# Kernel tuning notes

Measured on AMD Instinct MI355X. Metric: run time of the kernel, lower is better.

Reference implementation:

```python
import jax, jax.numpy as jnp
import numpy as np

N_NODES = 100000
N_EDGES = 1600000
D = 128

def setup_inputs() -> dict:
    key = jax.random.key(0)
    ks = jax.random.split(key, 6)
    x = jax.random.normal(ks[0], (N_NODES, D), dtype=jnp.float32)
    edge_src = jax.random.randint(ks[1], (N_EDGES,), 0, N_NODES, dtype=jnp.int32)
    edge_dst = jax.random.randint(ks[2], (N_EDGES,), 0, N_NODES, dtype=jnp.int32)
    # Glorot-ish scaling for 128x128 linears
    scale = 1.0 / np.sqrt(D)
    W1 = jax.random.normal(ks[3], (D, D), dtype=jnp.float32) * scale
    b1 = jnp.zeros((D,), dtype=jnp.float32)
    W2 = jax.random.normal(ks[4], (D, D), dtype=jnp.float32) * scale
    b2 = jnp.zeros((D,), dtype=jnp.float32)
    return {"x": x, "edge_src": edge_src, "edge_dst": edge_dst,
            "W1": W1, "b1": b1, "W2": W2, "b2": b2}

def reference(x, edge_src, edge_dst, W1, b1, W2, b2):
    # g.set_data('.hidden', data); g.apply(pre_mod): Linear + ReLU per node
    h = jax.nn.relu(x @ W1 + b1)                      # [N, D]
    # g.push(func=sum): each node's hidden becomes the sum of its
    # in-neighbors' hidden features (gather by src, scatter-add by dst).
    msgs = h[edge_src]                                # [E, D] irregular gather
    agg = jax.ops.segment_sum(msgs, edge_dst, num_segments=N_NODES)  # [N, D]
    # g.apply(post_mod): Linear per node; g.pop_data returns result
    out = agg @ W2 + b2                               # [N, D]
    return out
```

## Files before the change

### kernel.cpp

```cpp
#include <hip/hip_runtime.h>

#define D 128
#define NPB 256
#define NBMAX 512
#define BKCAP 8192
#define CHUNK 8192
#define OVF_CAP 8192

typedef __attribute__((ext_vector_type(8))) short short8x;
typedef __attribute__((ext_vector_type(4))) float f32x4;

__device__ inline unsigned int f2bf(float f) {
    unsigned int u = __builtin_bit_cast(unsigned int, f);
    return (u + 0x7fffu + ((u >> 16) & 1u)) >> 16;
}
__device__ inline float bflo(unsigned int v) {
    return __builtin_bit_cast(float, v << 16);
}
__device__ inline float bfhi(unsigned int v) {
    return __builtin_bit_cast(float, v & 0xffff0000u);
}
__device__ inline unsigned int pack2(float lo, float hi) {
    return f2bf(lo) | (f2bf(hi) << 16);
}

__global__ __launch_bounds__(256) void pack_w(
    const float* __restrict__ W1, const float* __restrict__ W2,
    uint4* __restrict__ pack, int* __restrict__ zero_area, int nz)
{
    if (blockIdx.x == 16) {
        for (int i = threadIdx.x; i < nz; i += 256) zero_area[i] = 0;
        return;
    }
    int e = blockIdx.x * 256 + threadIdx.x;
    const float* W = (e & 2048) ? W2 : W1;
    int f = (e >> 6) & 31, l = e & 63;
    int kt = f >> 3, nt = f & 7;
    int k0 = kt * 32 + (l >> 4) * 8;
    int col = nt * 16 + (l & 15);
    unsigned int v[8];
#pragma unroll
    for (int j = 0; j < 8; ++j) v[j] = f2bf(W[(size_t)(k0 + j) * D + col]);
    uint4 o;
    o.x = v[0] | (v[1] << 16);
    o.y = v[2] | (v[3] << 16);
    o.z = v[4] | (v[5] << 16);
    o.w = v[6] | (v[7] << 16);
    pack[e] = o;
}

__global__ __launch_bounds__(256) void build_gemm(
    const int* __restrict__ esrc, const int* __restrict__ edst,
    int* __restrict__ gfill, unsigned* __restrict__ pairs,
    int* __restrict__ ovf_cnt, int2* __restrict__ ovf_list, int E, int NB,
    int nscatter,
    const float* __restrict__ xin, const uint4* __restrict__ wpack,
    const float* __restrict__ b1, uint4* __restrict__ zout4, int n_rows)
{
    __shared__ __align__(16) char smem[65536];
    const int t = threadIdx.x;

    if (blockIdx.x < nscatter) {
        int* lcnt  = (int*)smem;
        int* lbase = lcnt + NBMAX;
        for (int b = t; b < NB; b += 256) lcnt[b] = 0;
        __syncthreads();
        int cb = blockIdx.x * CHUNK;
        int ce = min(E, cb + CHUNK);
        for (int i = cb + t; i < ce; i += 256)
            atomicAdd(&lcnt[edst[i] >> 8], 1);
        __syncthreads();
        for (int b = t; b < NB; b += 256) {
            int c = lcnt[b];
            lbase[b] = c ? atomicAdd(&gfill[b], c) : 0;
            lcnt[b] = 0;
        }
        __syncthreads();
        for (int i = cb + t; i < ce; i += 256) {
            int d = edst[i];
            int s = esrc[i];
            int b = d >> 8;
            int pos = lbase[b] + atomicAdd(&lcnt[b], 1);
            if (pos < BKCAP) {
                pairs[(size_t)b * BKCAP + pos] = ((unsigned)s << 8) | (unsigned)(d & 255);
            } else {
                int o = atomicAdd(ovf_cnt, 1);
                if (o < OVF_CAP) ovf_list[o] = make_int2(s, d);
            }
        }
        return;
    }

    uint4* ws  = (uint4*)smem;
    uint4* xs4 = ws + 2048;
    const int row0 = (blockIdx.x - nscatter) * 128;

#pragma unroll
    for (int i = 0; i < 8; ++i) ws[t + 256 * i] = wpack[t + 256 * i];

    const float4* g = (const float4*)xin;
#pragma unroll
    for (int i = 0; i < 8; ++i) {
        int c = t + 256 * i;
        int row = c >> 4, kc = c & 15;
        int grow = row0 + row;
        if (grow < n_rows) {
            float4 f0 = g[(size_t)grow * 32 + kc * 2];
            float4 f1 = g[(size_t)grow * 32 + kc * 2 + 1];
            uint4 v;
            v.x = pack2(f0.x, f0.y);
            v.y = pack2(f0.z, f0.w);
            v.z = pack2(f1.x, f1.y);
            v.w = pack2(f1.z, f1.w);
            xs4[row * 16 + (kc ^ (row & 7))] = v;
        }
    }
    __syncthreads();

    const int l = t & 63;
    const int w = t >> 6;
    const int l15 = l & 15;
    const int lk = l >> 4;
    const int arow0 = w * 32 + l15;
    const int arow1 = arow0 + 16;

    float bias1[8];
#pragma unroll
    for (int nt = 0; nt < 8; ++nt) bias1[nt] = b1[nt * 16 + l15];

    f32x4 acc1[2][8];
#pragma unroll
    for (int rt = 0; rt < 2; ++rt)
#pragma unroll
        for (int nt = 0; nt < 8; ++nt) acc1[rt][nt] = (f32x4){0.f, 0.f, 0.f, 0.f};

#pragma unroll
    for (int kt = 0; kt < 4; ++kt) {
        int kc0 = kt * 4 + lk;
        short8x a0 = *(const short8x*)&xs4[arow0 * 16 + (kc0 ^ (arow0 & 7))];
        short8x a1 = *(const short8x*)&xs4[arow1 * 16 + (kc0 ^ (arow1 & 7))];
#pragma unroll
        for (int nt = 0; nt < 8; ++nt) {
            short8x bf = *(const short8x*)&ws[(kt * 8 + nt) * 64 + l];
            acc1[0][nt] = __builtin_amdgcn_mfma_f32_16x16x32_bf16(a0, bf, acc1[0][nt], 0, 0, 0);
            acc1[1][nt] = __builtin_amdgcn_mfma_f32_16x16x32_bf16(a1, bf, acc1[1][nt], 0, 0, 0);
        }
    }

    unsigned short* hsu = (unsigned short*)xs4;
#pragma unroll
    for (int rt = 0; rt < 2; ++rt) {
#pragma unroll
        for (int nt = 0; nt < 8; ++nt) {
            int col = nt * 16 + l15;
            int ci = (col >> 3), ce2 = (col & 7);
#pragma unroll
            for (int r = 0; r < 4; ++r) {
                int rowl = w * 32 + rt * 16 + lk * 4 + r;
                float v = fmaxf(acc1[rt][nt][r] + bias1[nt], 0.f);
                hsu[(rowl * 16 + (ci ^ (rowl & 7))) * 8 + ce2] = (unsigned short)f2bf(v);
            }
        }
    }
    __syncthreads();

#pragma unroll
    for (int i = 0; i < 8; ++i) ws[t + 256 * i] = wpack[2048 + t + 256 * i];
    __syncthreads();

    f32x4 acc2[2][8];
#pragma unroll
    for (int rt = 0; rt < 2; ++rt)
#pragma unroll
        for (int nt = 0; nt < 8; ++nt) acc2[rt][nt] = (f32x4){0.f, 0.f, 0.f, 0.f};

#pragma unroll
    for (int kt = 0; kt < 4; ++kt) {
        int kc0 = kt * 4 + lk;
        short8x a0 = *(const short8x*)&xs4[arow0 * 16 + (kc0 ^ (arow0 & 7))];
        short8x a1 = *(const short8x*)&xs4[arow1 * 16 + (kc0 ^ (arow1 & 7))];
#pragma unroll
        for (int nt = 0; nt < 8; ++nt) {
            short8x bf = *(const short8x*)&ws[(kt * 8 + nt) * 64 + l];
            acc2[0][nt] = __builtin_amdgcn_mfma_f32_16x16x32_bf16(a0, bf, acc2[0][nt], 0, 0, 0);
            acc2[1][nt] = __builtin_amdgcn_mfma_f32_16x16x32_bf16(a1, bf, acc2[1][nt], 0, 0, 0);
        }
    }
    __syncthreads();

    unsigned short* zls = (unsigned short*)ws;
#pragma unroll
    for (int rt = 0; rt < 2; ++rt) {
#pragma unroll
        for (int nt = 0; nt < 8; ++nt) {
            int col = nt * 16 + l15;
#pragma unroll
            for (int r = 0; r < 4; ++r) {
                int rowl = w * 32 + rt * 16 + lk * 4 + r;
                zls[rowl * D + col] = (unsigned short)f2bf(acc2[rt][nt][r]);
            }
        }
    }
    __syncthreads();
    const uint4* zlsv = (const uint4*)zls;
#pragma unroll
    for (int i = 0; i < 8; ++i) {
        int c = t + 256 * i;
        int row = c >> 4, kc = c & 15;
        if (row0 + row < n_rows)
            zout4[(size_t)(row0 + row) * 16 + kc] = zlsv[c];
    }
}

__global__ __launch_bounds__(1024) void sort_pull(
    const unsigned* __restrict__ pairs, const int* __restrict__ gfill,
    const uint2* __restrict__ z2, const float* __restrict__ b2,
    float* __restrict__ out, int n_nodes)
{
    __shared__ int srcl[BKCAP];
    __shared__ int off[NPB + 1];
    __shared__ int fill[NPB];
    __shared__ int scanb[NPB];

    const int bkt = blockIdx.x;
    const int t = threadIdx.x;
    const size_t ebase = (size_t)bkt * BKCAP;
    const int ecnt = min(gfill[bkt], BKCAP);

    if (t < NPB) fill[t] = 0;
    __syncthreads();

    unsigned pv0, pv1, pv2, pv3, pv4, pv5, pv6, pv7;
#define LOADP(K, PV) { int i = t + (K) * 1024; \
        PV = (i < ecnt) ? pairs[ebase + i] : 0xFFFFFFFFu; \
        if (i < ecnt) atomicAdd(&fill[PV & 255], 1); }
    LOADP(0, pv0) LOADP(1, pv1) LOADP(2, pv2) LOADP(3, pv3)
    LOADP(4, pv4) LOADP(5, pv5) LOADP(6, pv6) LOADP(7, pv7)
#undef LOADP
    __syncthreads();

    if (t < NPB) scanb[t] = fill[t];
    __syncthreads();
    for (int s = 1; s < NPB; s <<= 1) {
        int add = 0;
        if (t < NPB && t >= s) add = scanb[t - s];
        __syncthreads();
        if (t < NPB) scanb[t] += add;
        __syncthreads();
    }
    if (t < NPB) {
        int c = fill[t];
        off[t] = scanb[t] - c;
        fill[t] = scanb[t] - c;
    }
    if (t == 0) off[NPB] = ecnt;
    __syncthreads();

#define SCATP(K, PV) { int i = t + (K) * 1024; \
        if (i < ecnt) { int pos = atomicAdd(&fill[PV & 255], 1); \
            srcl[pos] = (int)(PV >> 8); } }
    SCATP(0, pv0) SCATP(1, pv1) SCATP(2, pv2) SCATP(3, pv3)
    SCATP(4, pv4) SCATP(5, pv5) SCATP(6, pv6) SCATP(7, pv7)
#undef SCATP
    __syncthreads();

    const int grp = t >> 5;
    const int lane = t & 31;
    float4 bv = ((const float4*)b2)[lane];

    for (int ln = grp; ln < NPB; ln += 32) {
        int node = (bkt << 8) + ln;
        if (node >= n_nodes) break;
        int i = off[ln], end = off[ln + 1];

        float a0 = 0.f, a1 = 0.f, a2 = 0.f, a3 = 0.f;
        for (; i + 8 <= end; i += 8) {
            int s0 = srcl[i],     s1 = srcl[i + 1], s2 = srcl[i + 2], s3 = srcl[i + 3];
            int s4 = srcl[i + 4], s5 = srcl[i + 5], s6 = srcl[i + 6], s7 = srcl[i + 7];
            uint2 v0 = z2[(size_t)s0 * 32 + lane];
            uint2 v1 = z2[(size_t)s1 * 32 + lane];
            uint2 v2 = z2[(size_t)s2 * 32 + lane];
            uint2 v3 = z2[(size_t)s3 * 32 + lane];
            uint2 v4 = z2[(size_t)s4 * 32 + lane];
            uint2 v5 = z2[(size_t)s5 * 32 + lane];
            uint2 v6 = z2[(size_t)s6 * 32 + lane];
            uint2 v7 = z2[(size_t)s7 * 32 + lane];
            a0 += bflo(v0.x) + bflo(v1.x) + bflo(v2.x) + bflo(v3.x)
                + bflo(v4.x) + bflo(v5.x) + bflo(v6.x) + bflo(v7.x);
            a1 += bfhi(v0.x) + bfhi(v1.x) + bfhi(v2.x) + bfhi(v3.x)
                + bfhi(v4.x) + bfhi(v5.x) + bfhi(v6.x) + bfhi(v7.x);
            a2 += bflo(v0.y) + bflo(v1.y) + bflo(v2.y) + bflo(v3.y)
                + bflo(v4.y) + bflo(v5.y) + bflo(v6.y) + bflo(v7.y);
            a3 += bfhi(v0.y) + bfhi(v1.y) + bfhi(v2.y) + bfhi(v3.y)
                + bfhi(v4.y) + bfhi(v5.y) + bfhi(v6.y) + bfhi(v7.y);
        }
        if (i + 4 <= end) {
            int s0 = srcl[i], s1 = srcl[i + 1], s2 = srcl[i + 2], s3 = srcl[i + 3];
            uint2 v0 = z2[(size_t)s0 * 32 + lane];
            uint2 v1 = z2[(size_t)s1 * 32 + lane];
            uint2 v2 = z2[(size_t)s2 * 32 + lane];
            uint2 v3 = z2[(size_t)s3 * 32 + lane];
            a0 += bflo(v0.x) + bflo(v1.x) + bflo(v2.x) + bflo(v3.x);
            a1 += bfhi(v0.x) + bfhi(v1.x) + bfhi(v2.x) + bfhi(v3.x);
            a2 += bflo(v0.y) + bflo(v1.y) + bflo(v2.y) + bflo(v3.y);
            a3 += bfhi(v0.y) + bfhi(v1.y) + bfhi(v2.y) + bfhi(v3.y);
            i += 4;
        }
        for (; i < end; ++i) {
            uint2 v = z2[(size_t)srcl[i] * 32 + lane];
            a0 += bflo(v.x); a1 += bfhi(v.x);
            a2 += bflo(v.y); a3 += bfhi(v.y);
        }
        ((float4*)out)[(size_t)node * 32 + lane] =
            make_float4(a0 + bv.x, a1 + bv.y, a2 + bv.z, a3 + bv.w);
    }
}

__global__ __launch_bounds__(32) void ovf_f32(
    const int* __restrict__ ovf_cnt, const int2* __restrict__ ovf_list,
    const uint2* __restrict__ z2, float* __restrict__ out)
{
    int n = *ovf_cnt;
    if (n > OVF_CAP) n = OVF_CAP;
    int lane = threadIdx.x;
    for (int i = blockIdx.x; i < n; i += gridDim.x) {
        int2 sd = ovf_list[i];
        uint2 v = z2[(size_t)sd.x * 32 + lane];
        unsafeAtomicAdd(&out[(size_t)sd.y * D + lane * 4 + 0], bflo(v.x));
        unsafeAtomicAdd(&out[(size_t)sd.y * D + lane * 4 + 1], bfhi(v.x));
        unsafeAtomicAdd(&out[(size_t)sd.y * D + lane * 4 + 2], bflo(v.y));
        unsafeAtomicAdd(&out[(size_t)sd.y * D + lane * 4 + 3], bfhi(v.y));
    }
}

template <bool RELU>
__global__ __launch_bounds__(256) void gemm_bias_act(
    const float* xin, const float* __restrict__ W,
    const float* __restrict__ b, float* xout, int n_rows)
{
    __shared__ float Ws[D * D];
    __shared__ float xs[32 * D];
    const int t = threadIdx.x;
    const int row0 = blockIdx.x * 32;
    const float4* Wv = (const float4*)W;
    float4* Wsv = (float4*)Ws;
#pragma unroll
    for (int i = 0; i < 16; ++i) Wsv[t + 256 * i] = Wv[t + 256 * i];
    const float4* xv = (const float4*)xin;
    float4* xsv = (float4*)xs;
#pragma unroll
    for (int i = 0; i < 4; ++i) {
        int f4 = t + 256 * i;
        int row = row0 + (f4 >> 5);
        if (row < n_rows) xsv[f4] = xv[(size_t)row0 * 32 + f4];
    }
    __syncthreads();
    const int cg = t & 31;
    const int rg = t >> 5;
    float4 bias = ((const float4*)b)[cg];
    float4 acc[4];
#pragma unroll
    for (int ri = 0; ri < 4; ++ri) acc[ri] = make_float4(0.f, 0.f, 0.f, 0.f);
#pragma unroll 4
    for (int k = 0; k < D; k += 4) {
        float4 w0 = Wsv[(k + 0) * 32 + cg];
        float4 w1 = Wsv[(k + 1) * 32 + cg];
        float4 w2 = Wsv[(k + 2) * 32 + cg];
        float4 w3 = Wsv[(k + 3) * 32 + cg];
#pragma unroll
        for (int ri = 0; ri < 4; ++ri) {
            float4 xa = xsv[(rg + 8 * ri) * 32 + (k >> 2)];
            acc[ri].x = fmaf(xa.x, w0.x, fmaf(xa.y, w1.x, fmaf(xa.z, w2.x, fmaf(xa.w, w3.x, acc[ri].x))));
            acc[ri].y = fmaf(xa.x, w0.y, fmaf(xa.y, w1.y, fmaf(xa.z, w2.y, fmaf(xa.w, w3.y, acc[ri].y))));
            acc[ri].z = fmaf(xa.x, w0.z, fmaf(xa.y, w1.z, fmaf(xa.z, w2.z, fmaf(xa.w, w3.z, acc[ri].z))));
            acc[ri].w = fmaf(xa.x, w0.w, fmaf(xa.y, w1.w, fmaf(xa.z, w2.w, fmaf(xa.w, w3.w, acc[ri].w))));
        }
    }
#pragma unroll
    for (int ri = 0; ri < 4; ++ri) {
        int row = row0 + rg + 8 * ri;
        if (row >= n_rows) continue;
        float4 o;
        o.x = acc[ri].x + bias.x; o.y = acc[ri].y + bias.y;
        o.z = acc[ri].z + bias.z; o.w = acc[ri].w + bias.w;
        if (RELU) {
            o.x = fmaxf(o.x, 0.f); o.y = fmaxf(o.y, 0.f);
            o.z = fmaxf(o.z, 0.f); o.w = fmaxf(o.w, 0.f);
        }
        ((float4*)xout)[(size_t)row * 32 + cg] = o;
    }
}

__global__ __launch_bounds__(256) void zero_kernel(float4* p, int n4)
{
    int i = blockIdx.x * 256 + threadIdx.x;
    int stride = gridDim.x * 256;
    for (; i < n4; i += stride) p[i] = make_float4(0.f, 0.f, 0.f, 0.f);
}

__global__ __launch_bounds__(256) void scatter_kernel(
    const float* __restrict__ h, const int* __restrict__ esrc,
    const int* __restrict__ edst, float* __restrict__ agg, long n_items)
{
    long idx = (long)blockIdx.x * 256 + threadIdx.x;
    long stride = (long)gridDim.x * 256;
    for (; idx < n_items; idx += stride) {
        int e = (int)(idx >> 7);
        int c = (int)(idx & 127);
        int s = esrc[e];
        int d = edst[e];
        unsafeAtomicAdd(&agg[(size_t)d * D + c], h[(size_t)s * D + c]);
    }
}

extern "C" void kernel_launch(void* const* d_in, const int* in_sizes, int n_in,
                              void* d_out, int out_size, void* d_ws, size_t ws_size,
                              hipStream_t stream)
{
    const float* x    = (const float*)d_in[0];
    const int*   esrc = (const int*)d_in[1];
    const int*   edst = (const int*)d_in[2];
    const float* W1   = (const float*)d_in[3];
    const float* b1   = (const float*)d_in[4];
    const float* W2   = (const float*)d_in[5];
    const float* b2   = (const float*)d_in[6];
    float* out = (float*)d_out;

    const int N = in_sizes[0] / D;
    const int E = in_sizes[1];
    const int NB = (N + NPB - 1) / NPB;

    char* ws = (char*)d_ws;
    size_t off_z     = 0;
    size_t off_pairs = off_z + (size_t)N * 256;
    size_t off_gfill = (off_pairs + (size_t)NBMAX * BKCAP * 4 + 255) & ~(size_t)255;
    size_t off_ovfc  = off_gfill + NBMAX * 4;
    size_t off_ovfl  = off_ovfc + 16;
    size_t off_pack  = (off_ovfl + (size_t)OVF_CAP * 8 + 255) & ~(size_t)255;
    size_t need      = off_pack + 65536;

    const int gchunk  = (E + CHUNK - 1) / CHUNK;
    const int nblk128 = (N + 127) / 128;

    if (ws_size >= need && N <= NBMAX * NPB) {
        uint4*    z4    = (uint4*)(ws + off_z);
        unsigned* pairs = (unsigned*)(ws + off_pairs);
        int*      gfill = (int*)(ws + off_gfill);
        int*      ovfc  = (int*)(ws + off_ovfc);
        int2*     ovfl  = (int2*)(ws + off_ovfl);
        uint4*    pack  = (uint4*)(ws + off_pack);

        pack_w<<<17, 256, 0, stream>>>(W1, W2, pack, gfill, NBMAX + 4);

        build_gemm<<<gchunk + nblk128, 256, 0, stream>>>(
            esrc, edst, gfill, pairs, ovfc, ovfl, E, NB, gchunk,
            x, pack, b1, z4, N);

        sort_pull<<<NB, 1024, 0, stream>>>(
            pairs, gfill, (const uint2*)z4, b2, out, N);

        ovf_f32<<<8, 32, 0, stream>>>(ovfc, ovfl, (const uint2*)z4, out);
    } else {
        float* h = (float*)ws;
        const int nb32 = (N + 31) / 32;
        gemm_bias_act<true><<<nb32, 256, 0, stream>>>(x, W1, b1, h, N);
        zero_kernel<<<2048, 256, 0, stream>>>((float4*)out, N * D / 4);
        scatter_kernel<<<8192, 256, 0, stream>>>(h, esrc, edst, out, (long)E * D);
        gemm_bias_act<false><<<nb32, 256, 0, stream>>>(out, W2, b2, out, N);
    }
}
```

Measured before the change: 113.0 us.

## Split each sort_pull bucket across two blocks by node half

```diff
diff --git a/kernel.cpp b/kernel.cpp
--- a/kernel.cpp
+++ b/kernel.cpp
@@ -4,6 +4,7 @@
 #define NPB 256
 #define NBMAX 512
 #define BKCAP 8192
+#define SRCCAP 4096
 #define CHUNK 8192
 #define OVF_CAP 8192
 
@@ -215,50 +216,58 @@
 __global__ __launch_bounds__(1024) void sort_pull(
     const unsigned* __restrict__ pairs, const int* __restrict__ gfill,
     const uint2* __restrict__ z2, const float* __restrict__ b2,
-    float* __restrict__ out, int n_nodes)
-{
-    __shared__ int srcl[BKCAP];
-    __shared__ int off[NPB + 1];
-    __shared__ int fill[NPB];
-    __shared__ int scanb[NPB];
-
-    const int bkt = blockIdx.x;
+    float* __restrict__ out, int n_nodes,
+    int* __restrict__ ovf_cnt, int2* __restrict__ ovf_list)
+{
+    __shared__ int srcl[SRCCAP];
+    __shared__ int off[129];
+    __shared__ int fill[128];
+    __shared__ int scanb[128];
+
+    const int bkt  = blockIdx.x >> 1;
+    const int half = blockIdx.x & 1;
     const int t = threadIdx.x;
     const size_t ebase = (size_t)bkt * BKCAP;
     const int ecnt = min(gfill[bkt], BKCAP);
 
-    if (t < NPB) fill[t] = 0;
+    if (t < 128) fill[t] = 0;
     __syncthreads();
 
     unsigned pv0, pv1, pv2, pv3, pv4, pv5, pv6, pv7;
-#define LOADP(K, PV) { int i = t + (K) * 1024; \
-        PV = (i < ecnt) ? pairs[ebase + i] : 0xFFFFFFFFu; \
-        if (i < ecnt) atomicAdd(&fill[PV & 255], 1); }
+#define LOADP(K, PV) { int i = t + (K) * 1024; PV = 0xFFFFFFFFu; \
+        if (i < ecnt) { unsigned p = pairs[ebase + i]; \
+            if ((int)((p >> 7) & 1u) == half) { PV = p; atomicAdd(&fill[p & 127], 1); } } }
     LOADP(0, pv0) LOADP(1, pv1) LOADP(2, pv2) LOADP(3, pv3)
     LOADP(4, pv4) LOADP(5, pv5) LOADP(6, pv6) LOADP(7, pv7)
 #undef LOADP
     __syncthreads();
 
-    if (t < NPB) scanb[t] = fill[t];
-    __syncthreads();
-    for (int s = 1; s < NPB; s <<= 1) {
+    if (t < 128) scanb[t] = fill[t];
+    __syncthreads();
+    for (int s = 1; s < 128; s <<= 1) {
         int add = 0;
-        if (t < NPB && t >= s) add = scanb[t - s];
+        if (t < 128 && t >= s) add = scanb[t - s];
         __syncthreads();
-        if (t < NPB) scanb[t] += add;
+        if (t < 128) scanb[t] += add;
         __syncthreads();
     }
-    if (t < NPB) {
+    if (t < 128) {
         int c = fill[t];
         off[t] = scanb[t] - c;
         fill[t] = scanb[t] - c;
     }
-    if (t == 0) off[NPB] = ecnt;
-    __syncthreads();
-
-#define SCATP(K, PV) { int i = t + (K) * 1024; \
-        if (i < ecnt) { int pos = atomicAdd(&fill[PV & 255], 1); \
-            srcl[pos] = (int)(PV >> 8); } }
+    if (t == 0) off[128] = 0;
+    __syncthreads();
+    if (t == 127) off[128] = scanb[127];
+    __syncthreads();
+
+    const int nbase = (bkt << 8) + half * 128;
+
+#define SCATP(K, PV) { if (PV != 0xFFFFFFFFu) { \
+        int pos = atomicAdd(&fill[PV & 127], 1); \
+        if (pos < SRCCAP) srcl[pos] = (int)(PV >> 8); \
+        else { int o = atomicAdd(ovf_cnt, 1); \
+               if (o < OVF_CAP) ovf_list[o] = make_int2((int)(PV >> 8), nbase + (int)(PV & 127)); } } }
     SCATP(0, pv0) SCATP(1, pv1) SCATP(2, pv2) SCATP(3, pv3)
     SCATP(4, pv4) SCATP(5, pv5) SCATP(6, pv6) SCATP(7, pv7)
 #undef SCATP
@@ -268,10 +277,10 @@
     const int lane = t & 31;
     float4 bv = ((const float4*)b2)[lane];
 
-    for (int ln = grp; ln < NPB; ln += 32) {
-        int node = (bkt << 8) + ln;
+    for (int ln = grp; ln < 128; ln += 32) {
+        int node = nbase + ln;
         if (node >= n_nodes) break;
-        int i = off[ln], end = off[ln + 1];
+        int i = min(off[ln], SRCCAP), end = min(off[ln + 1], SRCCAP);
 
         float a0 = 0.f, a1 = 0.f, a2 = 0.f, a3 = 0.f;
         for (; i + 8 <= end; i += 8) {
@@ -456,8 +465,8 @@
             esrc, edst, gfill, pairs, ovfc, ovfl, E, NB, gchunk,
             x, pack, b1, z4, N);
 
-        sort_pull<<<NB, 1024, 0, stream>>>(
-            pairs, gfill, (const uint2*)z4, b2, out, N);
+        sort_pull<<<NB * 2, 1024, 0, stream>>>(
+            pairs, gfill, (const uint2*)z4, b2, out, N, ovfc, ovfl);
 
         ovf_f32<<<8, 32, 0, stream>>>(ovfc, ovfl, (const uint2*)z4, out);
     } else {
```

Result: no change. 115.0 us (+1.8%).
